# Optimization experiments

Measured on AMD Instinct MI355X. Metric: run time of the kernel, lower is better.

## Reference

```python
import jax, jax.numpy as jnp
import numpy as np

SCALES = (4, 8, 8)
PAD = 2
TOTAL = 256  # prod(SCALES) == frame shift
INDENT = PAD * TOTAL
BN_EPS = 1e-3  # keras BatchNormalization default


def _bn(x, g, b, m, v):
    return (x - m) * jax.lax.rsqrt(v + BN_EPS) * g + b


def _conv1d_valid(x, w):
    # x: [B, T, Cin], w: [K, Cin, Cout]
    return jax.lax.conv_general_dilated(x, w, (1,), 'VALID',
                                         dimension_numbers=('NWC', 'WIO', 'NWC'))


def _mel_conv_same(x, w):
    # per-mel-bin shared 1D conv along time. x: [B, T, M], w: [K]
    B, T, M = x.shape
    lhs = x.transpose(0, 2, 1).reshape(B * M, T, 1)
    rhs = w.reshape(-1, 1, 1)
    y = jax.lax.conv_general_dilated(lhs, rhs, (1,), 'SAME',
                                     dimension_numbers=('NWC', 'WIO', 'NWC'))
    return y.reshape(B, M, T).transpose(0, 2, 1)


def _gru(x, Wx, Wh, bx, bh):
    # keras GRUCell (reset_after=True): gate order z, r, h; h' = z*h + (1-z)*hh
    xp = x @ Wx + bx  # [B, T, 3H], input projection hoisted out of the scan
    H = Wh.shape[0]
    h0 = jnp.zeros((x.shape[0], H), x.dtype)

    def step(h, xt):
        rp = h @ Wh + bh
        xz, xr, xh = jnp.split(xt, 3, axis=-1)
        rz, rr, rh = jnp.split(rp, 3, axis=-1)
        z = jax.nn.sigmoid(xz + rz)
        r = jax.nn.sigmoid(xr + rr)
        hh = jnp.tanh(xh + r * rh)
        hn = z * h + (1.0 - z) * hh
        return hn, hn

    _, ys = jax.lax.scan(step, h0, xp.transpose(1, 0, 2))
    return ys.transpose(1, 0, 2)


def setup_inputs() -> dict:
    key = jax.random.key(0)
    ks = iter(jax.random.split(key, 64))
    B, T_MEL, M, C, H, R = 4, 44, 80, 128, 512, 10
    T_UP = TOTAL * (T_MEL - 2 * PAD)  # 10240
    s = 0.05
    d = {}
    d['audios'] = jax.random.normal(next(ks), (B, T_UP + 1), jnp.float32)
    d['mels'] = jax.random.normal(next(ks), (B, T_MEL, M), jnp.float32)
    d['w_mel0'] = jnp.full((2 * SCALES[0] + 1,), 1.0 / (2 * SCALES[0] + 1), jnp.float32)
    d['w_mel1'] = jnp.full((2 * SCALES[1] + 1,), 1.0 / (2 * SCALES[1] + 1), jnp.float32)
    d['w_mel2'] = jnp.full((2 * SCALES[2] + 1,), 1.0 / (2 * SCALES[2] + 1), jnp.float32)
    d['mr_conv0_w'] = jax.random.normal(next(ks), (5, M, C), jnp.float32) * s
    d['mr_bn0_g'] = jax.random.uniform(next(ks), (C,), jnp.float32, 0.5, 1.5)
    d['mr_bn0_b'] = jax.random.normal(next(ks), (C,), jnp.float32) * s
    d['mr_bn0_m'] = jnp.zeros((C,), jnp.float32)
    d['mr_bn0_v'] = jnp.ones((C,), jnp.float32)
    d['r_w1'] = jax.random.normal(next(ks), (R, C, C), jnp.float32) * s
    d['r_bn1_g'] = jax.random.uniform(next(ks), (R, C), jnp.float32, 0.5, 1.5)
    d['r_bn1_b'] = jax.random.normal(next(ks), (R, C), jnp.float32) * s
    d['r_bn1_m'] = jnp.zeros((R, C), jnp.float32)
    d['r_bn1_v'] = jnp.ones((R, C), jnp.float32)
    d['r_w2'] = jax.random.normal(next(ks), (R, C, C), jnp.float32) * s
    d['r_bn2_g'] = jax.random.uniform(next(ks), (R, C), jnp.float32, 0.5, 1.5)
    d['r_bn2_b'] = jax.random.normal(next(ks), (R, C), jnp.float32) * s
    d['r_bn2_m'] = jnp.zeros((R, C), jnp.float32)
    d['r_bn2_v'] = jnp.ones((R, C), jnp.float32)
    d['mr_out_w'] = jax.random.normal(next(ks), (C, C), jnp.float32) * s
    d['mr_out_b'] = jnp.zeros((C,), jnp.float32)
    A4 = C // 4  # 32
    d['Wi'] = jax.random.normal(next(ks), (1 + M + A4, H), jnp.float32) * s
    d['bi'] = jnp.zeros((H,), jnp.float32)
    d['Wx0'] = jax.random.normal(next(ks), (H, 3 * H), jnp.float32) * s
    d['Wh0'] = jax.random.normal(next(ks), (H, 3 * H), jnp.float32) * s
    d['bx0'] = jnp.zeros((3 * H,), jnp.float32)
    d['bh0'] = jnp.zeros((3 * H,), jnp.float32)
    d['Wx1'] = jax.random.normal(next(ks), (H + A4, 3 * H), jnp.float32) * s
    d['Wh1'] = jax.random.normal(next(ks), (H, 3 * H), jnp.float32) * s
    d['bx1'] = jnp.zeros((3 * H,), jnp.float32)
    d['bh1'] = jnp.zeros((3 * H,), jnp.float32)
    d['Wd0'] = jax.random.normal(next(ks), (H + A4, H), jnp.float32) * s
    d['bd0'] = jnp.zeros((H,), jnp.float32)
    d['Wd1'] = jax.random.normal(next(ks), (H + A4, H), jnp.float32) * s
    d['bd1'] = jnp.zeros((H,), jnp.float32)
    d['Wp'] = jax.random.normal(next(ks), (H, 30), jnp.float32) * s
    d['bp'] = jnp.zeros((30,), jnp.float32)
    return d


def reference(audios, mels, w_mel0, w_mel1, w_mel2,
              mr_conv0_w, mr_bn0_g, mr_bn0_b, mr_bn0_m, mr_bn0_v,
              r_w1, r_bn1_g, r_bn1_b, r_bn1_m, r_bn1_v,
              r_w2, r_bn2_g, r_bn2_b, r_bn2_m, r_bn2_v,
              mr_out_w, mr_out_b, Wi, bi,
              Wx0, Wh0, bx0, bh0, Wx1, Wh1, bx1, bh1,
              Wd0, bd0, Wd1, bd1, Wp, bp):
    # ---- UpsampleNet mel branch: nearest upsample + smoothing conv per scale ----
    x = mels
    for w, scale in zip((w_mel0, w_mel1, w_mel2), SCALES):
        x = jnp.repeat(x, scale, axis=1)
        x = _mel_conv_same(x, w)
    mels_up = x[:, INDENT:-INDENT, :]  # [B, T_up, 80]

    # ---- UpsampleNet aux branch: MelResNet (inference BN) + nearest upsample ----
    a = jax.nn.relu(_bn(_conv1d_valid(mels, mr_conv0_w),
                        mr_bn0_g, mr_bn0_b, mr_bn0_m, mr_bn0_v))
    for i in range(r_w1.shape[0]):
        y = jax.nn.relu(_bn(a @ r_w1[i], r_bn1_g[i], r_bn1_b[i], r_bn1_m[i], r_bn1_v[i]))
        y = _bn(y @ r_w2[i], r_bn2_g[i], r_bn2_b[i], r_bn2_m[i], r_bn2_v[i])
        a = a + y
    a = a @ mr_out_w + mr_out_b
    aux = jnp.repeat(a, TOTAL, axis=1)  # [B, T_up, 128]
    a0, a1, a2, a3 = jnp.split(aux, 4, axis=-1)

    # ---- WaveRNN teacher-forced trunk ----
    x = jnp.concatenate([audios[:, :-1, None], mels_up, a0], axis=-1)
    x = x @ Wi + bi  # [B, T_up, 512]
    x = _gru(x, Wx0, Wh0, bx0, bh0) + x
    x = _gru(jnp.concatenate([x, a1], axis=-1), Wx1, Wh1, bx1, bh1) + x
    x = jax.nn.relu(jnp.concatenate([x, a2], axis=-1) @ Wd0 + bd0) + x
    x = jax.nn.relu(jnp.concatenate([x, a3], axis=-1) @ Wd1 + bd1) + x
    logits = x @ Wp + bp  # [B, T_up, 30] (MoL parameters)
    return logits
```

## Files before the change

kernel.cpp:

```cpp
#include <hip/hip_runtime.h>
#include <hip/hip_bf16.h>

#define T_SEQ 10240
#define GRU_W 8

typedef short bf16x8 __attribute__((ext_vector_type(8)));
typedef float f32x4 __attribute__((ext_vector_type(4)));

__device__ __forceinline__ float bf2f(unsigned short u) {
    return __uint_as_float(((unsigned int)u) << 16);
}

__global__ void upsample_kernel(const float* __restrict__ in, float* __restrict__ out,
                                const float* __restrict__ wk,
                                int B, int Tin, int Tout, int shift, int taps)
{
    int idx = blockIdx.x * blockDim.x + threadIdx.x;
    int total = B * Tout * 80;
    if (idx >= total) return;
    int m = idx % 80;
    int r = idx / 80;
    int t = r % Tout;
    int b = r / Tout;
    int s = taps >> 1;
    float acc = 0.f;
    for (int d = -s; d <= s; ++d) {
        int i = t + d;
        if (i >= 0 && i < Tout)
            acc += in[((size_t)b * Tin + (i >> shift)) * 80 + m] * wk[d + s];
    }
    out[idx] = acc;
}

__global__ __launch_bounds__(128) void conv0_kernel(
    const float* __restrict__ mels, const float* __restrict__ w,
    const float* __restrict__ g, const float* __restrict__ b,
    const float* __restrict__ m_, const float* __restrict__ v_,
    float* __restrict__ a)
{
    __shared__ float xin[400];
    int bt = blockIdx.x;
    int bb = bt / 40, t = bt % 40;
    int c = threadIdx.x;
    for (int idx = c; idx < 400; idx += 128)
        xin[idx] = mels[((size_t)bb * 44 + t + idx / 80) * 80 + (idx % 80)];
    __syncthreads();
    float s = 0.f;
    for (int q = 0; q < 400; ++q) s += xin[q] * w[q * 128 + c];
    s = (s - m_[c]) * rsqrtf(v_[c] + 1e-3f) * g[c] + b[c];
    a[bt * 128 + c] = fmaxf(s, 0.f);
}

__global__ __launch_bounds__(128) void resblock_kernel(
    const float* __restrict__ W1, const float* __restrict__ W2,
    const float* __restrict__ g1, const float* __restrict__ b1,
    const float* __restrict__ m1, const float* __restrict__ v1,
    const float* __restrict__ g2, const float* __restrict__ b2,
    const float* __restrict__ m2, const float* __restrict__ v2,
    float* __restrict__ a)
{
    __shared__ float ain[128], y1[128];
    int tok = blockIdx.x;
    int c = threadIdx.x;
    ain[c] = a[tok * 128 + c];
    __syncthreads();
    float s = 0.f;
    #pragma unroll 8
    for (int k = 0; k < 128; ++k) s += ain[k] * W1[k * 128 + c];
    s = (s - m1[c]) * rsqrtf(v1[c] + 1e-3f) * g1[c] + b1[c];
    y1[c] = fmaxf(s, 0.f);
    __syncthreads();
    float s2 = 0.f;
    #pragma unroll 8
    for (int k = 0; k < 128; ++k) s2 += y1[k] * W2[k * 128 + c];
    s2 = (s2 - m2[c]) * rsqrtf(v2[c] + 1e-3f) * g2[c] + b2[c];
    a[tok * 128 + c] = ain[c] + s2;
}

__global__ __launch_bounds__(128) void outmat_kernel(
    const float* __restrict__ W, const float* __restrict__ bias,
    const float* __restrict__ a, float* __restrict__ out)
{
    __shared__ float ain[128];
    int tok = blockIdx.x;
    int c = threadIdx.x;
    ain[c] = a[tok * 128 + c];
    __syncthreads();
    float s = 0.f;
    #pragma unroll 8
    for (int k = 0; k < 128; ++k) s += ain[k] * W[k * 128 + c];
    out[tok * 128 + c] = s + bias[c];
}

__device__ __forceinline__ float fetchA(int mode, int row, int k, int K,
    const float* audio, const float* melsup, const float* cond, const float* xA)
{
    if (k >= K) return 0.f;
    int b = row / T_SEQ;
    int t = row - b * T_SEQ;
    if (mode == 0) {
        if (k == 0) return audio[(size_t)b * (T_SEQ + 1) + t];
        if (k < 81) return melsup[((size_t)b * 11264 + 512 + t) * 80 + (k - 1)];
        return cond[((size_t)b * 40 + (t >> 8)) * 128 + (k - 81)];
    }
    if (k < 512) return xA[(size_t)row * 512 + k];
    int co = (mode == 2) ? 32 : (mode == 3) ? 64 : 96;
    return cond[((size_t)b * 40 + (t >> 8)) * 128 + co + (k - 512)];
}

__global__ __launch_bounds__(256) void gemm_big(
    int mode, int N, int K,
    const float* __restrict__ W, const float* __restrict__ bias1,
    const float* __restrict__ bias2,
    const float* __restrict__ audio, const float* __restrict__ melsup,
    const float* __restrict__ cond, const float* __restrict__ xA,
    const float* __restrict__ resid, float* __restrict__ outF,
    __hip_bfloat16* __restrict__ outB)
{
    __shared__ float As[16][68];
    __shared__ float Bs[16][68];
    const int tid = threadIdx.x;
    const int row0 = blockIdx.y * 64;
    const int col0 = blockIdx.x * 64;
    const int tx = tid & 15, ty = tid >> 4;
    float acc[4][4] = {};
    const int nkt = (K + 15) >> 4;
    for (int kt = 0; kt < nkt; ++kt) {
        const int kb = kt << 4;
        #pragma unroll
        for (int l = 0; l < 4; ++l) {
            int k = (tid >> 6) + l * 4;
            int m = tid & 63;
            float bv = 0.f;
            if (kb + k < K) bv = W[(size_t)(kb + k) * N + col0 + m];
            Bs[k][m] = bv;
        }
        if (mode != 0) {
            int m = tid >> 2, kq = tid & 3;
            int row = row0 + m;
            int k = kb + kq * 4;
            if (k + 3 < 512) {
                float4 v = *reinterpret_cast<const float4*>(xA + (size_t)row * 512 + k);
                As[kq * 4 + 0][m] = v.x; As[kq * 4 + 1][m] = v.y;
                As[kq * 4 + 2][m] = v.z; As[kq * 4 + 3][m] = v.w;
            } else {
                #pragma unroll
                for (int i = 0; i < 4; ++i)
                    As[kq * 4 + i][m] = fetchA(mode, row, k + i, K, audio, melsup, cond, xA);
            }
        } else {
            #pragma unroll
            for (int l = 0; l < 4; ++l) {
                int k = (tid >> 6) + l * 4;
                int m = tid & 63;
                As[k][m] = fetchA(0, row0 + m, kb + k, K, audio, melsup, cond, xA);
            }
        }
        __syncthreads();
        #pragma unroll
        for (int k = 0; k < 16; ++k) {
            float a0 = As[k][(ty << 2) + 0], a1 = As[k][(ty << 2) + 1];
            float a2 = As[k][(ty << 2) + 2], a3 = As[k][(ty << 2) + 3];
            float b0 = Bs[k][(tx << 2) + 0], b1 = Bs[k][(tx << 2) + 1];
            float b2 = Bs[k][(tx << 2) + 2], b3 = Bs[k][(tx << 2) + 3];
            acc[0][0] += a0 * b0; acc[0][1] += a0 * b1; acc[0][2] += a0 * b2; acc[0][3] += a0 * b3;
            acc[1][0] += a1 * b0; acc[1][1] += a1 * b1; acc[1][2] += a1 * b2; acc[1][3] += a1 * b3;
            acc[2][0] += a2 * b0; acc[2][1] += a2 * b1; acc[2][2] += a2 * b2; acc[2][3] += a2 * b3;
            acc[3][0] += a3 * b0; acc[3][1] += a3 * b1; acc[3][2] += a3 * b2; acc[3][3] += a3 * b3;
        }
        __syncthreads();
    }
    #pragma unroll
    for (int i = 0; i < 4; ++i) {
        int row = row0 + (ty << 2) + i;
        #pragma unroll
        for (int jt = 0; jt < 4; ++jt) {
            int col = col0 + (tx << 2) + jt;
            float v = acc[i][jt] + bias1[col];
            if (bias2 && col < 1024) v += bias2[col];
            if (mode == 0) {
                outF[(size_t)row * N + col] = v;
            } else if (mode <= 2) {
                outB[(size_t)row * 1536 + col] = __float2bfloat16(v);
            } else {
                v = fmaxf(v, 0.f) + resid[(size_t)row * 512 + col];
                outF[(size_t)row * 512 + col] = v;
            }
        }
    }
}

__global__ __launch_bounds__(256) void pack_wh_kernel(const float* __restrict__ Wh,
                                                      unsigned short* __restrict__ out)
{
    int gid = blockIdx.x * 256 + threadIdx.x;
    int l = gid & 63;
    int idx = gid >> 6;
    int kt = idx & 15; idx >>= 4;
    int g = idx % 3;
    int ww = idx / 3;
    int wg = ww >> 2, w = ww & 3;
    int n = g * 512 + wg * 64 + w * 16 + (l & 15);
    int k0 = kt * 32 + (l >> 4) * 8;
    unsigned short* dst = out + (size_t)gid * 8;
    #pragma unroll
    for (int i = 0; i < 8; ++i) {
        __hip_bfloat16 hv = __float2bfloat16(Wh[(size_t)(k0 + i) * 1536 + n]);
        dst[i] = *reinterpret_cast<unsigned short*>(&hv);
    }
}

__global__ __launch_bounds__(256, 1) void gru_mfma8(
    const unsigned short* __restrict__ wpack,
    const float* __restrict__ bh,
    const __hip_bfloat16* __restrict__ xp,
    float* __restrict__ xio,
    unsigned int* __restrict__ hpair,
    int T)
{
    __shared__ alignas(16) unsigned short h_sh[2][16 * 512];

    const int tid = threadIdx.x;
    const int wg = blockIdx.x;
    const int w = tid >> 6;
    const int l = tid & 63;

    bf16x8 wf[3][16];
    {
        const bf16x8* wp = reinterpret_cast<const bf16x8*>(wpack);
        const int wbase = (wg * 4 + w) * 3 * 1024;
        #pragma unroll
        for (int g = 0; g < 3; ++g)
            #pragma unroll
            for (int kt = 0; kt < 16; ++kt)
                wf[g][kt] = wp[wbase + (g * 16 + kt) * 64 + l];
    }

    {
        uint4* z = reinterpret_cast<uint4*>(&h_sh[0][0]);
        #pragma unroll
        for (int i = 0; i < 8; ++i) z[tid + 256 * i] = make_uint4(0, 0, 0, 0);
    }

    const int j = wg * 64 + w * 16 + (l & 15);
    const float bhh = bh[1024 + j];
    float hprev[4] = {0.f, 0.f, 0.f, 0.f};
    float xz_c[4], xr_c[4], xh_c[4], xv_c[4];
    if (l < 16) {
        #pragma unroll
        for (int b = 0; b < 4; ++b) {
            const size_t rb = (size_t)b * T;
            xz_c[b] = bf2f(*reinterpret_cast<const unsigned short*>(xp + rb * 1536 + j));
            xr_c[b] = bf2f(*reinterpret_cast<const unsigned short*>(xp + rb * 1536 + 512 + j));
            xh_c[b] = bf2f(*reinterpret_cast<const unsigned short*>(xp + rb * 1536 + 1024 + j));
            xv_c[b] = xio[rb * 512 + j];
        }
    }
    __syncthreads();

    const unsigned long long* hp64 = reinterpret_cast<const unsigned long long*>(hpair);
    const int pb = tid >> 6;
    const int pchunk = (tid & 63) ^ (pb & 7);

    for (int t = 0; t < T; ++t) {
        const int cur = t & 1, nxt = cur ^ 1;

        const unsigned long long* src = hp64 + (size_t)cur * 1024 + tid * 4;
        const unsigned tg = (unsigned)t & 0xffffu;
        unsigned long long u0 = __hip_atomic_load(src + 0, __ATOMIC_RELAXED, __HIP_MEMORY_SCOPE_AGENT);
        unsigned long long u1 = __hip_atomic_load(src + 1, __ATOMIC_RELAXED, __HIP_MEMORY_SCOPE_AGENT);
        unsigned long long u2 = __hip_atomic_load(src + 2, __ATOMIC_RELAXED, __HIP_MEMORY_SCOPE_AGENT);
        unsigned long long u3 = __hip_atomic_load(src + 3, __ATOMIC_RELAXED, __HIP_MEMORY_SCOPE_AGENT);
        while ((((unsigned)(u0 >> 16) & 0xffffu) != tg) | ((unsigned)(u0 >> 48) != tg) |
               (((unsigned)(u1 >> 16) & 0xffffu) != tg) | ((unsigned)(u1 >> 48) != tg) |
               (((unsigned)(u2 >> 16) & 0xffffu) != tg) | ((unsigned)(u2 >> 48) != tg) |
               (((unsigned)(u3 >> 16) & 0xffffu) != tg) | ((unsigned)(u3 >> 48) != tg)) {
            __builtin_amdgcn_s_sleep(1);
            u0 = __hip_atomic_load(src + 0, __ATOMIC_RELAXED, __HIP_MEMORY_SCOPE_AGENT);
            u1 = __hip_atomic_load(src + 1, __ATOMIC_RELAXED, __HIP_MEMORY_SCOPE_AGENT);
            u2 = __hip_atomic_load(src + 2, __ATOMIC_RELAXED, __HIP_MEMORY_SCOPE_AGENT);
            u3 = __hip_atomic_load(src + 3, __ATOMIC_RELAXED, __HIP_MEMORY_SCOPE_AGENT);
        }
        {
            uint4 wv;
            wv.x = (unsigned)(u0 & 0xffffull) | ((unsigned)((u0 >> 32) & 0xffffull) << 16);
            wv.y = (unsigned)(u1 & 0xffffull) | ((unsigned)((u1 >> 32) & 0xffffull) << 16);
            wv.z = (unsigned)(u2 & 0xffffull) | ((unsigned)((u2 >> 32) & 0xffffull) << 16);
            wv.w = (unsigned)(u3 & 0xffffull) | ((unsigned)((u3 >> 32) & 0xffffull) << 16);
            *reinterpret_cast<uint4*>(
                reinterpret_cast<char*>(&h_sh[cur][0]) + pb * 1024 + pchunk * 16) = wv;
        }
        __syncthreads();

        f32x4 acc0 = {0, 0, 0, 0}, acc1 = {0, 0, 0, 0}, acc2 = {0, 0, 0, 0};
        const int rb = l & 15, q = l >> 4;
        const char* hb = reinterpret_cast<const char*>(&h_sh[cur][0]);
        #pragma unroll
        for (int kt = 0; kt < 16; ++kt) {
            bf16x8 afr = *reinterpret_cast<const bf16x8*>(
                hb + rb * 1024 + ((((kt * 4 + q) ^ (rb & 7))) << 4));
            acc0 = __builtin_amdgcn_mfma_f32_16x16x32_bf16(afr, wf[0][kt], acc0, 0, 0, 0);
            acc1 = __builtin_amdgcn_mfma_f32_16x16x32_bf16(afr, wf[1][kt], acc1, 0, 0, 0);
            acc2 = __builtin_amdgcn_mfma_f32_16x16x32_bf16(afr, wf[2][kt], acc2, 0, 0, 0);
        }

        if (l < 16) {
            float hn[4];
            #pragma unroll
            for (int b = 0; b < 4; ++b) {
                float z = 1.f / (1.f + __expf(-(xz_c[b] + acc0[b])));
                float r = 1.f / (1.f + __expf(-(xr_c[b] + acc1[b])));
                float e2 = __expf(-2.f * (xh_c[b] + r * (acc2[b] + bhh)));
                float hh = (1.f - e2) / (1.f + e2);
                hn[b] = z * hprev[b] + (1.f - z) * hh;
                hprev[b] = hn[b];
            }
            if (t + 1 < T) {
                const unsigned ptag = (unsigned)((t + 1) & 0xffff) << 16;
                #pragma unroll
                for (int b = 0; b < 4; ++b) {
                    __hip_bfloat16 hb16 = __float2bfloat16(hn[b]);
                    __hip_atomic_store(hpair + (size_t)nxt * 2048 + b * 512 + j,
                                       ptag | (unsigned)*reinterpret_cast<unsigned short*>(&hb16),
                                       __ATOMIC_RELAXED, __HIP_MEMORY_SCOPE_AGENT);
                }
            }
            #pragma unroll
            for (int b = 0; b < 4; ++b)
                xio[((size_t)b * T + t) * 512 + j] = xv_c[b] + hn[b];
            if (t + 1 < T) {
                #pragma unroll
                for (int b = 0; b < 4; ++b) {
                    const size_t rb2 = (size_t)b * T + t + 1;
                    xz_c[b] = bf2f(*reinterpret_cast<const unsigned short*>(xp + rb2 * 1536 + j));
                    xr_c[b] = bf2f(*reinterpret_cast<const unsigned short*>(xp + rb2 * 1536 + 512 + j));
                    xh_c[b] = bf2f(*reinterpret_cast<const unsigned short*>(xp + rb2 * 1536 + 1024 + j));
                    xv_c[b] = xio[rb2 * 512 + j];
                }
            }
        }
    }
}

__global__ __launch_bounds__(256) void wp_kernel(
    const float* __restrict__ x, const float* __restrict__ Wp,
    const float* __restrict__ bp, float* __restrict__ out)
{
    int r = threadIdx.x >> 5, c = threadIdx.x & 31;
    size_t row = (size_t)blockIdx.x * 8 + r;
    if (c >= 30) return;
    const float* xr = x + row * 512;
    float acc = 0.f;
    #pragma unroll 8
    for (int k = 0; k < 512; ++k) acc += xr[k] * Wp[k * 30 + c];
    out[row * 30 + c] = acc + bp[c];
}

extern "C" void kernel_launch(void* const* d_in, const int* in_sizes, int n_in,
                              void* d_out, int out_size, void* d_ws, size_t ws_size,
                              hipStream_t stream)
{
    const float* audios = (const float*)d_in[0];
    const float* mels   = (const float*)d_in[1];
    const float* w_mel0 = (const float*)d_in[2];
    const float* w_mel1 = (const float*)d_in[3];
    const float* w_mel2 = (const float*)d_in[4];
    const float* conv0w = (const float*)d_in[5];
    const float* bn0g = (const float*)d_in[6];
    const float* bn0b = (const float*)d_in[7];
    const float* bn0m = (const float*)d_in[8];
    const float* bn0v = (const float*)d_in[9];
    const float* r_w1   = (const float*)d_in[10];
    const float* r_bn1g = (const float*)d_in[11];
    const float* r_bn1b = (const float*)d_in[12];
    const float* r_bn1m = (const float*)d_in[13];
    const float* r_bn1v = (const float*)d_in[14];
    const float* r_w2   = (const float*)d_in[15];
    const float* r_bn2g = (const float*)d_in[16];
    const float* r_bn2b = (const float*)d_in[17];
    const float* r_bn2m = (const float*)d_in[18];
    const float* r_bn2v = (const float*)d_in[19];
    const float* mr_out_w = (const float*)d_in[20];
    const float* mr_out_b = (const float*)d_in[21];
    const float* Wi = (const float*)d_in[22];
    const float* bi = (const float*)d_in[23];
    const float* Wx0 = (const float*)d_in[24];
    const float* Wh0 = (const float*)d_in[25];
    const float* bx0 = (const float*)d_in[26];
    const float* bh0 = (const float*)d_in[27];
    const float* Wx1 = (const float*)d_in[28];
    const float* Wh1 = (const float*)d_in[29];
    const float* bx1 = (const float*)d_in[30];
    const float* bh1 = (const float*)d_in[31];
    const float* Wd0 = (const float*)d_in[32];
    const float* bd0 = (const float*)d_in[33];
    const float* Wd1 = (const float*)d_in[34];
    const float* bd1 = (const float*)d_in[35];
    const float* Wp = (const float*)d_in[36];
    const float* bp = (const float*)d_in[37];

    char* ws = (char*)d_ws;
    size_t off = 0;
    auto alloc = [&](size_t n) { size_t r = off; off += (n + 255) & ~(size_t)255; return r; };
    const size_t M = 4 * (size_t)T_SEQ;
    size_t xp_off = alloc(M * 1536 * 2);
    size_t x_off  = alloc(M * 512 * 4);
    size_t s1_off = alloc((size_t)4 * 176 * 80 * 4);
    size_t s2_off = alloc((size_t)4 * 1408 * 80 * 4);
    size_t s3_off = alloc((size_t)4 * 11264 * 80 * 4);
    size_t ca_off = alloc((size_t)160 * 128 * 4);
    size_t cf_off = alloc((size_t)160 * 128 * 4);
    size_t wp0_off = alloc((size_t)98304 * 8 * 2);
    size_t wp1_off = alloc((size_t)98304 * 8 * 2);
    size_t hp_off  = alloc(2 * 2048 * 4);

    __hip_bfloat16* xp = (__hip_bfloat16*)(ws + xp_off);
    float* x3   = (float*)(ws + xp_off);
    float* xbuf = (float*)(ws + x_off);
    float* st1  = (float*)(ws + s1_off);
    float* st2  = (float*)(ws + s2_off);
    float* st3  = (float*)(ws + s3_off);
    float* conda = (float*)(ws + ca_off);
    float* condf = (float*)(ws + cf_off);
    unsigned short* wpack0 = (unsigned short*)(ws + wp0_off);
    unsigned short* wpack1 = (unsigned short*)(ws + wp1_off);
    unsigned int* hpair = (unsigned int*)(ws + hp_off);
    float* outp = (float*)d_out;

    pack_wh_kernel<<<384, 256, 0, stream>>>(Wh0, wpack0);
    pack_wh_kernel<<<384, 256, 0, stream>>>(Wh1, wpack1);

    {
        int tot1 = 4 * 176 * 80;
        upsample_kernel<<<(tot1 + 255) / 256, 256, 0, stream>>>(mels, st1, w_mel0, 4, 44, 176, 2, 9);
        int tot2 = 4 * 1408 * 80;
        upsample_kernel<<<(tot2 + 255) / 256, 256, 0, stream>>>(st1, st2, w_mel1, 4, 176, 1408, 3, 17);
        int tot3 = 4 * 11264 * 80;
        upsample_kernel<<<(tot3 + 255) / 256, 256, 0, stream>>>(st2, st3, w_mel2, 4, 1408, 11264, 3, 17);
    }
    conv0_kernel<<<160, 128, 0, stream>>>(mels, conv0w, bn0g, bn0b, bn0m, bn0v, conda);
    for (int i = 0; i < 10; ++i) {
        resblock_kernel<<<160, 128, 0, stream>>>(
            r_w1 + (size_t)i * 128 * 128, r_w2 + (size_t)i * 128 * 128,
            r_bn1g + i * 128, r_bn1b + i * 128, r_bn1m + i * 128, r_bn1v + i * 128,
            r_bn2g + i * 128, r_bn2b + i * 128, r_bn2m + i * 128, r_bn2v + i * 128,
            conda);
    }
    outmat_kernel<<<160, 128, 0, stream>>>(mr_out_w, mr_out_b, conda, condf);

    dim3 blk(256);
    gemm_big<<<dim3(8, 640), blk, 0, stream>>>(0, 512, 113, Wi, bi, nullptr,
        audios, st3, condf, nullptr, nullptr, xbuf, nullptr);
    gemm_big<<<dim3(24, 640), blk, 0, stream>>>(1, 1536, 512, Wx0, bx0, bh0,
        nullptr, nullptr, condf, xbuf, nullptr, nullptr, xp);
    hipMemsetAsync(ws + hp_off, 0, 2 * 2048 * 4, stream);
    gru_mfma8<<<GRU_W, 256, 0, stream>>>(wpack0, bh0, xp, xbuf, hpair, T_SEQ);
    gemm_big<<<dim3(24, 640), blk, 0, stream>>>(2, 1536, 544, Wx1, bx1, bh1,
        nullptr, nullptr, condf, xbuf, nullptr, nullptr, xp);
    hipMemsetAsync(ws + hp_off, 0, 2 * 2048 * 4, stream);
    gru_mfma8<<<GRU_W, 256, 0, stream>>>(wpack1, bh1, xp, xbuf, hpair, T_SEQ);
    gemm_big<<<dim3(8, 640), blk, 0, stream>>>(3, 512, 544, Wd0, bd0, nullptr,
        nullptr, nullptr, condf, xbuf, xbuf, x3, nullptr);
    gemm_big<<<dim3(8, 640), blk, 0, stream>>>(4, 512, 544, Wd1, bd1, nullptr,
        nullptr, nullptr, condf, x3, x3, xbuf, nullptr);
    wp_kernel<<<5120, 256, 0, stream>>>(xbuf, Wp, bp, outp);
}
```

Before: 48.35 ms.

## Fuse both GRU layers into one pipelined persistent kernel with in-loop input projection

Replaces the two sequential GRU launches and their two big input-projection GEMMs with a single 16-block persistent kernel. Layer 0 and layer 1 run concurrently, with layer 1 consuming layer 0 outputs through a tagged ring buffer and a progress counter that bounds the lag. Each block adds four extra waves that compute the x@Wx projection per timestep with MFMA. The per-frame conditioning part of layer 1 is precomputed by a small kernel. This removes the GEMM passes and the xp round-trip through memory and overlaps the two recurrences. In exchange the per-step critical path gets longer, there is more block-to-block synchronisation, and layer-0 outputs are now rounded to bf16.

```diff
diff --git a/kernel.cpp b/kernel.cpp
--- a/kernel.cpp
+++ b/kernel.cpp
@@ -2,13 +2,16 @@
 #include <hip/hip_bf16.h>
 
 #define T_SEQ 10240
-#define GRU_W 8
 
 typedef short bf16x8 __attribute__((ext_vector_type(8)));
 typedef float f32x4 __attribute__((ext_vector_type(4)));
 
 __device__ __forceinline__ float bf2f(unsigned short u) {
     return __uint_as_float(((unsigned int)u) << 16);
+}
+__device__ __forceinline__ unsigned short f2bf(float f) {
+    __hip_bfloat16 h = __float2bfloat16(f);
+    return *reinterpret_cast<unsigned short*>(&h);
 }
 
 __global__ void upsample_kernel(const float* __restrict__ in, float* __restrict__ out,
@@ -104,14 +107,13 @@
         return cond[((size_t)b * 40 + (t >> 8)) * 128 + (k - 81)];
     }
     if (k < 512) return xA[(size_t)row * 512 + k];
-    int co = (mode == 2) ? 32 : (mode == 3) ? 64 : 96;
+    int co = (mode == 3) ? 64 : 96;
     return cond[((size_t)b * 40 + (t >> 8)) * 128 + co + (k - 512)];
 }
 
 __global__ __launch_bounds__(256) void gemm_big(
     int mode, int N, int K,
     const float* __restrict__ W, const float* __restrict__ bias1,
-    const float* __restrict__ bias2,
     const float* __restrict__ audio, const float* __restrict__ melsup,
     const float* __restrict__ cond, const float* __restrict__ xA,
     const float* __restrict__ resid, float* __restrict__ outF,
@@ -177,11 +179,8 @@
         for (int jt = 0; jt < 4; ++jt) {
             int col = col0 + (tx << 2) + jt;
             float v = acc[i][jt] + bias1[col];
-            if (bias2 && col < 1024) v += bias2[col];
             if (mode == 0) {
-                outF[(size_t)row * N + col] = v;
-            } else if (mode <= 2) {
-                outB[(size_t)row * 1536 + col] = __float2bfloat16(v);
+                outB[(size_t)row * 512 + col] = __float2bfloat16(v);
             } else {
                 v = fmaxf(v, 0.f) + resid[(size_t)row * 512 + col];
                 outF[(size_t)row * 512 + col] = v;
@@ -190,127 +189,232 @@
     }
 }
 
-__global__ __launch_bounds__(256) void pack_wh_kernel(const float* __restrict__ Wh,
-                                                      unsigned short* __restrict__ out)
-{
-    int gid = blockIdx.x * 256 + threadIdx.x;
-    int l = gid & 63;
-    int idx = gid >> 6;
+__global__ __launch_bounds__(256) void pack_w_kernel(const float* __restrict__ Wh,
+                                                     const float* __restrict__ Wx,
+                                                     unsigned short* __restrict__ out)
+{
+    int F = blockIdx.x * 256 + threadIdx.x;
+    int l = F & 63;
+    int idx = F >> 6;
     int kt = idx & 15; idx >>= 4;
-    int g = idx % 3;
-    int ww = idx / 3;
-    int wg = ww >> 2, w = ww & 3;
-    int n = g * 512 + wg * 64 + w * 16 + (l & 15);
+    int g = idx % 3; idx /= 3;
+    int w = idx & 7;
+    int wg = idx >> 3;
+    const float* src = (w < 4) ? Wh : Wx;
+    int uw = w & 3;
+    int n = g * 512 + wg * 64 + uw * 16 + (l & 15);
     int k0 = kt * 32 + (l >> 4) * 8;
-    unsigned short* dst = out + (size_t)gid * 8;
+    unsigned short* dst = out + (size_t)F * 8;
     #pragma unroll
-    for (int i = 0; i < 8; ++i) {
-        __hip_bfloat16 hv = __float2bfloat16(Wh[(size_t)(k0 + i) * 1536 + n]);
-        dst[i] = *reinterpret_cast<unsigned short*>(&hv);
-    }
-}
-
-__global__ __launch_bounds__(256, 1) void gru_mfma8(
+    for (int i = 0; i < 8; ++i)
+        dst[i] = f2bf(src[(size_t)(k0 + i) * 1536 + n]);
+}
+
+__global__ __launch_bounds__(256) void xa1_kernel(const float* __restrict__ Wx1,
+                                                  const float* __restrict__ bx1,
+                                                  const float* __restrict__ bh1,
+                                                  const float* __restrict__ cond,
+                                                  float* __restrict__ xa1)
+{
+    int idx = blockIdx.x * 256 + threadIdx.x;
+    if (idx >= 245760) return;
+    int n = idx % 1536;
+    int bf = idx / 1536;
+    float s = bx1[n] + (n < 1024 ? bh1[n] : 0.f);
+    const float* a = cond + (size_t)bf * 128 + 32;
+    #pragma unroll 8
+    for (int k = 0; k < 32; ++k) s += a[k] * Wx1[(size_t)(512 + k) * 1536 + n];
+    xa1[idx] = s;
+}
+
+__global__ __launch_bounds__(512, 1) void gru_fused(
     const unsigned short* __restrict__ wpack,
-    const float* __restrict__ bh,
-    const __hip_bfloat16* __restrict__ xp,
+    const float* __restrict__ bx0, const float* __restrict__ bh0,
+    const float* __restrict__ bh1,
+    const float* __restrict__ xa1,
+    const __hip_bfloat16* __restrict__ xb16,
     float* __restrict__ xio,
-    unsigned int* __restrict__ hpair,
+    unsigned int* __restrict__ hr0,
+    unsigned int* __restrict__ hr1,
+    unsigned int* __restrict__ x1r,
+    unsigned int* __restrict__ prog,
     int T)
 {
-    __shared__ alignas(16) unsigned short h_sh[2][16 * 512];
+    __shared__ alignas(16) unsigned short h_sh[16 * 512];
+    __shared__ alignas(16) unsigned short x_sh[3][16 * 512];
+    __shared__ alignas(16) float accx[4][16][3][4];
+    __shared__ alignas(16) float xab[4][16][3][4];
 
     const int tid = threadIdx.x;
-    const int wg = blockIdx.x;
-    const int w = tid >> 6;
-    const int l = tid & 63;
+    const int layer = blockIdx.x >> 3, wg = blockIdx.x & 7;
+    const int w = tid >> 6, l = tid & 63;
+    const bool ish = (w < 4);
+    const int uw = w & 3;
 
     bf16x8 wf[3][16];
     {
         const bf16x8* wp = reinterpret_cast<const bf16x8*>(wpack);
-        const int wbase = (wg * 4 + w) * 3 * 1024;
+        const size_t base = (size_t)layer * 196608 + (size_t)((wg * 8 + w) * 3) * 16 * 64;
         #pragma unroll
         for (int g = 0; g < 3; ++g)
             #pragma unroll
             for (int kt = 0; kt < 16; ++kt)
-                wf[g][kt] = wp[wbase + (g * 16 + kt) * 64 + l];
+                wf[g][kt] = wp[base + (g * 16 + kt) * 64 + l];
     }
 
     {
-        uint4* z = reinterpret_cast<uint4*>(&h_sh[0][0]);
-        #pragma unroll
-        for (int i = 0; i < 8; ++i) z[tid + 256 * i] = make_uint4(0, 0, 0, 0);
-    }
-
-    const int j = wg * 64 + w * 16 + (l & 15);
-    const float bhh = bh[1024 + j];
+        uint4* z1 = reinterpret_cast<uint4*>(h_sh);
+        for (int i = tid; i < 1024; i += 512) z1[i] = make_uint4(0, 0, 0, 0);
+        uint4* z2 = reinterpret_cast<uint4*>(&x_sh[0][0]);
+        for (int i = tid; i < 3072; i += 512) z2[i] = make_uint4(0, 0, 0, 0);
+    }
+
+    const int j = wg * 64 + uw * 16 + (l & 15);
+    float bhh = 0.f;
     float hprev[4] = {0.f, 0.f, 0.f, 0.f};
-    float xz_c[4], xr_c[4], xh_c[4], xv_c[4];
-    if (l < 16) {
+    if (ish && l < 16)
+        bhh = (layer == 0) ? bh0[1024 + j] : bh1[1024 + j];
+    __syncthreads();
+
+    if (ish && l < 16 && layer == 0) {
         #pragma unroll
         for (int b = 0; b < 4; ++b) {
-            const size_t rb = (size_t)b * T;
-            xz_c[b] = bf2f(*reinterpret_cast<const unsigned short*>(xp + rb * 1536 + j));
-            xr_c[b] = bf2f(*reinterpret_cast<const unsigned short*>(xp + rb * 1536 + 512 + j));
-            xh_c[b] = bf2f(*reinterpret_cast<const unsigned short*>(xp + rb * 1536 + 1024 + j));
-            xv_c[b] = xio[rb * 512 + j];
-        }
-    }
-    __syncthreads();
-
-    const unsigned long long* hp64 = reinterpret_cast<const unsigned long long*>(hpair);
-    const int pb = tid >> 6;
-    const int pchunk = (tid & 63) ^ (pb & 7);
+            xab[w][l][0][b] = bx0[j] + bh0[j];
+            xab[w][l][1][b] = bx0[512 + j] + bh0[512 + j];
+            xab[w][l][2][b] = bx0[1024 + j];
+        }
+    }
+
+    const int xc = tid & 255;
+    const int xb = xc >> 6, xch = xc & 63;
+    uint4 xhold = make_uint4(0, 0, 0, 0);
+    if (!ish && layer == 0) {
+        uint4 v0 = *reinterpret_cast<const uint4*>(
+            reinterpret_cast<const unsigned short*>(xb16) + ((size_t)xb * T) * 512 + xch * 8);
+        *reinterpret_cast<uint4*>(
+            reinterpret_cast<char*>(&x_sh[0][0]) + xb * 1024 + ((xch ^ (xb & 7))) * 16) = v0;
+        int t1 = (T > 1) ? 1 : 0;
+        xhold = *reinterpret_cast<const uint4*>(
+            reinterpret_cast<const unsigned short*>(xb16) + ((size_t)xb * T + t1) * 512 + xch * 8);
+    }
+
+    unsigned int* hr = layer ? hr1 : hr0;
+    const unsigned long long* hr64 = reinterpret_cast<const unsigned long long*>(hr);
+    const unsigned long long* xr64 = reinterpret_cast<const unsigned long long*>(x1r);
 
     for (int t = 0; t < T; ++t) {
-        const int cur = t & 1, nxt = cur ^ 1;
-
-        const unsigned long long* src = hp64 + (size_t)cur * 1024 + tid * 4;
-        const unsigned tg = (unsigned)t & 0xffffu;
-        unsigned long long u0 = __hip_atomic_load(src + 0, __ATOMIC_RELAXED, __HIP_MEMORY_SCOPE_AGENT);
-        unsigned long long u1 = __hip_atomic_load(src + 1, __ATOMIC_RELAXED, __HIP_MEMORY_SCOPE_AGENT);
-        unsigned long long u2 = __hip_atomic_load(src + 2, __ATOMIC_RELAXED, __HIP_MEMORY_SCOPE_AGENT);
-        unsigned long long u3 = __hip_atomic_load(src + 3, __ATOMIC_RELAXED, __HIP_MEMORY_SCOPE_AGENT);
-        while ((((unsigned)(u0 >> 16) & 0xffffu) != tg) | ((unsigned)(u0 >> 48) != tg) |
-               (((unsigned)(u1 >> 16) & 0xffffu) != tg) | ((unsigned)(u1 >> 48) != tg) |
-               (((unsigned)(u2 >> 16) & 0xffffu) != tg) | ((unsigned)(u2 >> 48) != tg) |
-               (((unsigned)(u3 >> 16) & 0xffffu) != tg) | ((unsigned)(u3 >> 48) != tg)) {
-            __builtin_amdgcn_s_sleep(1);
-            u0 = __hip_atomic_load(src + 0, __ATOMIC_RELAXED, __HIP_MEMORY_SCOPE_AGENT);
-            u1 = __hip_atomic_load(src + 1, __ATOMIC_RELAXED, __HIP_MEMORY_SCOPE_AGENT);
-            u2 = __hip_atomic_load(src + 2, __ATOMIC_RELAXED, __HIP_MEMORY_SCOPE_AGENT);
-            u3 = __hip_atomic_load(src + 3, __ATOMIC_RELAXED, __HIP_MEMORY_SCOPE_AGENT);
-        }
-        {
+        const int cur = t & 1;
+        const int xbuf = t % 3;
+        unsigned pg0 = 0;
+
+        if (ish) {
+            if (layer == 0 && l < 16)
+                pg0 = __hip_atomic_load(prog + (l & 7) * 16, __ATOMIC_RELAXED, __HIP_MEMORY_SCOPE_AGENT);
+            const unsigned long long* src = hr64 + (size_t)cur * 1024 + tid * 4;
+            const unsigned tg = (unsigned)t & 0xffffu;
+            unsigned long long u0 = __hip_atomic_load(src + 0, __ATOMIC_RELAXED, __HIP_MEMORY_SCOPE_AGENT);
+            unsigned long long u1 = __hip_atomic_load(src + 1, __ATOMIC_RELAXED, __HIP_MEMORY_SCOPE_AGENT);
+            unsigned long long u2 = __hip_atomic_load(src + 2, __ATOMIC_RELAXED, __HIP_MEMORY_SCOPE_AGENT);
+            unsigned long long u3 = __hip_atomic_load(src + 3, __ATOMIC_RELAXED, __HIP_MEMORY_SCOPE_AGENT);
+            while ((((unsigned)(u0 >> 16) & 0xffffu) != tg) | ((unsigned)(u0 >> 48) != tg) |
+                   (((unsigned)(u1 >> 16) & 0xffffu) != tg) | ((unsigned)(u1 >> 48) != tg) |
+                   (((unsigned)(u2 >> 16) & 0xffffu) != tg) | ((unsigned)(u2 >> 48) != tg) |
+                   (((unsigned)(u3 >> 16) & 0xffffu) != tg) | ((unsigned)(u3 >> 48) != tg)) {
+                __builtin_amdgcn_s_sleep(1);
+                u0 = __hip_atomic_load(src + 0, __ATOMIC_RELAXED, __HIP_MEMORY_SCOPE_AGENT);
+                u1 = __hip_atomic_load(src + 1, __ATOMIC_RELAXED, __HIP_MEMORY_SCOPE_AGENT);
+                u2 = __hip_atomic_load(src + 2, __ATOMIC_RELAXED, __HIP_MEMORY_SCOPE_AGENT);
+                u3 = __hip_atomic_load(src + 3, __ATOMIC_RELAXED, __HIP_MEMORY_SCOPE_AGENT);
+            }
             uint4 wv;
             wv.x = (unsigned)(u0 & 0xffffull) | ((unsigned)((u0 >> 32) & 0xffffull) << 16);
             wv.y = (unsigned)(u1 & 0xffffull) | ((unsigned)((u1 >> 32) & 0xffffull) << 16);
             wv.z = (unsigned)(u2 & 0xffffull) | ((unsigned)((u2 >> 32) & 0xffffull) << 16);
             wv.w = (unsigned)(u3 & 0xffffull) | ((unsigned)((u3 >> 32) & 0xffffull) << 16);
             *reinterpret_cast<uint4*>(
-                reinterpret_cast<char*>(&h_sh[cur][0]) + pb * 1024 + pchunk * 16) = wv;
+                reinterpret_cast<char*>(h_sh) + (tid >> 6) * 1024 +
+                (((tid & 63) ^ ((tid >> 6) & 7))) * 16) = wv;
+        } else {
+            if (layer == 0) {
+                *reinterpret_cast<uint4*>(
+                    reinterpret_cast<char*>(&x_sh[(t + 1) % 3][0]) + xb * 1024 +
+                    ((xch ^ (xb & 7))) * 16) = xhold;
+                int tn = (t + 2 < T) ? t + 2 : T - 1;
+                xhold = *reinterpret_cast<const uint4*>(
+                    reinterpret_cast<const unsigned short*>(xb16) +
+                    ((size_t)xb * T + tn) * 512 + xch * 8);
+            } else {
+                const unsigned long long* src = xr64 + (size_t)(t & 31) * 1024 + xc * 4;
+                const unsigned tg = (unsigned)(t + 1) & 0xffffu;
+                unsigned long long u0 = __hip_atomic_load(src + 0, __ATOMIC_RELAXED, __HIP_MEMORY_SCOPE_AGENT);
+                unsigned long long u1 = __hip_atomic_load(src + 1, __ATOMIC_RELAXED, __HIP_MEMORY_SCOPE_AGENT);
+                unsigned long long u2 = __hip_atomic_load(src + 2, __ATOMIC_RELAXED, __HIP_MEMORY_SCOPE_AGENT);
+                unsigned long long u3 = __hip_atomic_load(src + 3, __ATOMIC_RELAXED, __HIP_MEMORY_SCOPE_AGENT);
+                while ((((unsigned)(u0 >> 16) & 0xffffu) != tg) | ((unsigned)(u0 >> 48) != tg) |
+                       (((unsigned)(u1 >> 16) & 0xffffu) != tg) | ((unsigned)(u1 >> 48) != tg) |
+                       (((unsigned)(u2 >> 16) & 0xffffu) != tg) | ((unsigned)(u2 >> 48) != tg) |
+                       (((unsigned)(u3 >> 16) & 0xffffu) != tg) | ((unsigned)(u3 >> 48) != tg)) {
+                    __builtin_amdgcn_s_sleep(1);
+                    u0 = __hip_atomic_load(src + 0, __ATOMIC_RELAXED, __HIP_MEMORY_SCOPE_AGENT);
+                    u1 = __hip_atomic_load(src + 1, __ATOMIC_RELAXED, __HIP_MEMORY_SCOPE_AGENT);
+                    u2 = __hip_atomic_load(src + 2, __ATOMIC_RELAXED, __HIP_MEMORY_SCOPE_AGENT);
+                    u3 = __hip_atomic_load(src + 3, __ATOMIC_RELAXED, __HIP_MEMORY_SCOPE_AGENT);
+                }
+                uint4 wv;
+                wv.x = (unsigned)(u0 & 0xffffull) | ((unsigned)((u0 >> 32) & 0xffffull) << 16);
+                wv.y = (unsigned)(u1 & 0xffffull) | ((unsigned)((u1 >> 32) & 0xffffull) << 16);
+                wv.z = (unsigned)(u2 & 0xffffull) | ((unsigned)((u2 >> 32) & 0xffffull) << 16);
+                wv.w = (unsigned)(u3 & 0xffffull) | ((unsigned)((u3 >> 32) & 0xffffull) << 16);
+                *reinterpret_cast<uint4*>(
+                    reinterpret_cast<char*>(&x_sh[xbuf][0]) + xb * 1024 +
+                    ((xch ^ (xb & 7))) * 16) = wv;
+            }
         }
         __syncthreads();
 
-        f32x4 acc0 = {0, 0, 0, 0}, acc1 = {0, 0, 0, 0}, acc2 = {0, 0, 0, 0};
+        const char* A = ish ? reinterpret_cast<const char*>(h_sh)
+                            : reinterpret_cast<const char*>(&x_sh[xbuf][0]);
+        f32x4 a0 = {0, 0, 0, 0}, a1 = {0, 0, 0, 0}, a2 = {0, 0, 0, 0};
         const int rb = l & 15, q = l >> 4;
-        const char* hb = reinterpret_cast<const char*>(&h_sh[cur][0]);
         #pragma unroll
         for (int kt = 0; kt < 16; ++kt) {
             bf16x8 afr = *reinterpret_cast<const bf16x8*>(
-                hb + rb * 1024 + ((((kt * 4 + q) ^ (rb & 7))) << 4));
-            acc0 = __builtin_amdgcn_mfma_f32_16x16x32_bf16(afr, wf[0][kt], acc0, 0, 0, 0);
-            acc1 = __builtin_amdgcn_mfma_f32_16x16x32_bf16(afr, wf[1][kt], acc1, 0, 0, 0);
-            acc2 = __builtin_amdgcn_mfma_f32_16x16x32_bf16(afr, wf[2][kt], acc2, 0, 0, 0);
-        }
-
-        if (l < 16) {
-            float hn[4];
+                A + rb * 1024 + ((((kt * 4 + q) ^ (rb & 7))) << 4));
+            a0 = __builtin_amdgcn_mfma_f32_16x16x32_bf16(afr, wf[0][kt], a0, 0, 0, 0);
+            a1 = __builtin_amdgcn_mfma_f32_16x16x32_bf16(afr, wf[1][kt], a1, 0, 0, 0);
+            a2 = __builtin_amdgcn_mfma_f32_16x16x32_bf16(afr, wf[2][kt], a2, 0, 0, 0);
+        }
+        if (!ish && l < 16) {
+            *reinterpret_cast<f32x4*>(&accx[uw][l][0][0]) = a0;
+            *reinterpret_cast<f32x4*>(&accx[uw][l][1][0]) = a1;
+            *reinterpret_cast<f32x4*>(&accx[uw][l][2][0]) = a2;
+        }
+        __syncthreads();
+
+        if (ish && l < 16) {
+            if (layer == 1 && (t & 255) == 0) {
+                const int f = t >> 8;
+                #pragma unroll
+                for (int b = 0; b < 4; ++b) {
+                    const size_t base = (size_t)(b * 40 + f) * 1536;
+                    xab[w][l][0][b] = xa1[base + j];
+                    xab[w][l][1][b] = xa1[base + 512 + j];
+                    xab[w][l][2][b] = xa1[base + 1024 + j];
+                }
+            }
+            float hn[4], xv[4];
             #pragma unroll
             for (int b = 0; b < 4; ++b) {
-                float z = 1.f / (1.f + __expf(-(xz_c[b] + acc0[b])));
-                float r = 1.f / (1.f + __expf(-(xr_c[b] + acc1[b])));
-                float e2 = __expf(-2.f * (xh_c[b] + r * (acc2[b] + bhh)));
+                const unsigned short xu = *reinterpret_cast<const unsigned short*>(
+                    reinterpret_cast<const char*>(&x_sh[xbuf][0]) + b * 1024 +
+                    (((j >> 3) ^ (b & 7)) << 4) + (j & 7) * 2);
+                xv[b] = bf2f(xu);
+                float xz_ = accx[w][l][0][b] + xab[w][l][0][b];
+                float xr_ = accx[w][l][1][b] + xab[w][l][1][b];
+                float xh_ = accx[w][l][2][b] + xab[w][l][2][b];
+                float z = 1.f / (1.f + __expf(-(xz_ + a0[b])));
+                float r = 1.f / (1.f + __expf(-(xr_ + a1[b])));
+                float e2 = __expf(-2.f * (xh_ + r * (a2[b] + bhh)));
                 float hh = (1.f - e2) / (1.f + e2);
                 hn[b] = z * hprev[b] + (1.f - z) * hh;
                 hprev[b] = hn[b];
@@ -318,25 +422,29 @@
             if (t + 1 < T) {
                 const unsigned ptag = (unsigned)((t + 1) & 0xffff) << 16;
                 #pragma unroll
-                for (int b = 0; b < 4; ++b) {
-                    __hip_bfloat16 hb16 = __float2bfloat16(hn[b]);
-                    __hip_atomic_store(hpair + (size_t)nxt * 2048 + b * 512 + j,
-                                       ptag | (unsigned)*reinterpret_cast<unsigned short*>(&hb16),
+                for (int b = 0; b < 4; ++b)
+                    __hip_atomic_store(hr + (size_t)((t + 1) & 1) * 2048 + b * 512 + j,
+                                       ptag | (unsigned)f2bf(hn[b]),
                                        __ATOMIC_RELAXED, __HIP_MEMORY_SCOPE_AGENT);
+            }
+            if (layer == 0) {
+                while ((int)t - (int)pg0 > 24) {
+                    __builtin_amdgcn_s_sleep(8);
+                    pg0 = __hip_atomic_load(prog + (l & 7) * 16, __ATOMIC_RELAXED, __HIP_MEMORY_SCOPE_AGENT);
                 }
-            }
-            #pragma unroll
-            for (int b = 0; b < 4; ++b)
-                xio[((size_t)b * T + t) * 512 + j] = xv_c[b] + hn[b];
-            if (t + 1 < T) {
+                const unsigned xtag = (unsigned)((t + 1) & 0xffff) << 16;
                 #pragma unroll
-                for (int b = 0; b < 4; ++b) {
-                    const size_t rb2 = (size_t)b * T + t + 1;
-                    xz_c[b] = bf2f(*reinterpret_cast<const unsigned short*>(xp + rb2 * 1536 + j));
-                    xr_c[b] = bf2f(*reinterpret_cast<const unsigned short*>(xp + rb2 * 1536 + 512 + j));
-                    xh_c[b] = bf2f(*reinterpret_cast<const unsigned short*>(xp + rb2 * 1536 + 1024 + j));
-                    xv_c[b] = xio[rb2 * 512 + j];
-                }
+                for (int b = 0; b < 4; ++b)
+                    __hip_atomic_store(x1r + (size_t)(t & 31) * 2048 + b * 512 + j,
+                                       xtag | (unsigned)f2bf(xv[b] + hn[b]),
+                                       __ATOMIC_RELAXED, __HIP_MEMORY_SCOPE_AGENT);
+            } else {
+                #pragma unroll
+                for (int b = 0; b < 4; ++b)
+                    xio[((size_t)b * T + t) * 512 + j] = xv[b] + hn[b];
+                if (w == 0 && l == 0)
+                    __hip_atomic_store(prog + wg * 16, (unsigned)t,
+                                       __ATOMIC_RELAXED, __HIP_MEMORY_SCOPE_AGENT);
             }
         }
     }
@@ -403,41 +511,41 @@
     size_t off = 0;
     auto alloc = [&](size_t n) { size_t r = off; off += (n + 255) & ~(size_t)255; return r; };
     const size_t M = 4 * (size_t)T_SEQ;
-    size_t xp_off = alloc(M * 1536 * 2);
-    size_t x_off  = alloc(M * 512 * 4);
+    size_t x3_off  = alloc(M * 512 * 4);
+    size_t xio_off = alloc(M * 512 * 4);
+    size_t xb_off  = alloc(M * 512 * 2);
     size_t s1_off = alloc((size_t)4 * 176 * 80 * 4);
     size_t s2_off = alloc((size_t)4 * 1408 * 80 * 4);
     size_t s3_off = alloc((size_t)4 * 11264 * 80 * 4);
     size_t ca_off = alloc((size_t)160 * 128 * 4);
     size_t cf_off = alloc((size_t)160 * 128 * 4);
-    size_t wp0_off = alloc((size_t)98304 * 8 * 2);
-    size_t wp1_off = alloc((size_t)98304 * 8 * 2);
-    size_t hp_off  = alloc(2 * 2048 * 4);
-
-    __hip_bfloat16* xp = (__hip_bfloat16*)(ws + xp_off);
-    float* x3   = (float*)(ws + xp_off);
-    float* xbuf = (float*)(ws + x_off);
+    size_t wp_off = alloc((size_t)2 * 196608 * 8 * 2);
+    size_t xa_off = alloc((size_t)245760 * 4);
+    size_t rg_off = alloc(16384 + 16384 + 262144 + 512);
+
+    float* x3   = (float*)(ws + x3_off);
+    float* xio  = (float*)(ws + xio_off);
+    __hip_bfloat16* xb16 = (__hip_bfloat16*)(ws + xb_off);
     float* st1  = (float*)(ws + s1_off);
     float* st2  = (float*)(ws + s2_off);
     float* st3  = (float*)(ws + s3_off);
     float* conda = (float*)(ws + ca_off);
     float* condf = (float*)(ws + cf_off);
-    unsigned short* wpack0 = (unsigned short*)(ws + wp0_off);
-    unsigned short* wpack1 = (unsigned short*)(ws + wp1_off);
-    unsigned int* hpair = (unsigned int*)(ws + hp_off);
+    unsigned short* wpack = (unsigned short*)(ws + wp_off);
+    float* xa1 = (float*)(ws + xa_off);
+    unsigned int* hr0 = (unsigned int*)(ws + rg_off);
+    unsigned int* hr1 = (unsigned int*)(ws + rg_off + 16384);
+    unsigned int* x1r = (unsigned int*)(ws + rg_off + 32768);
+    unsigned int* prog = (unsigned int*)(ws + rg_off + 32768 + 262144);
     float* outp = (float*)d_out;
 
-    pack_wh_kernel<<<384, 256, 0, stream>>>(Wh0, wpack0);
-    pack_wh_kernel<<<384, 256, 0, stream>>>(Wh1, wpack1);
-
-    {
-        int tot1 = 4 * 176 * 80;
-        upsample_kernel<<<(tot1 + 255) / 256, 256, 0, stream>>>(mels, st1, w_mel0, 4, 44, 176, 2, 9);
-        int tot2 = 4 * 1408 * 80;
-        upsample_kernel<<<(tot2 + 255) / 256, 256, 0, stream>>>(st1, st2, w_mel1, 4, 176, 1408, 3, 17);
-        int tot3 = 4 * 11264 * 80;
-        upsample_kernel<<<(tot3 + 255) / 256, 256, 0, stream>>>(st2, st3, w_mel2, 4, 1408, 11264, 3, 17);
-    }
+    pack_w_kernel<<<768, 256, 0, stream>>>(Wh0, Wx0, wpack);
+    pack_w_kernel<<<768, 256, 0, stream>>>(Wh1, Wx1, wpack + (size_t)196608 * 8);
+
+    upsample_kernel<<<(4 * 176 * 80 + 255) / 256, 256, 0, stream>>>(mels, st1, w_mel0, 4, 44, 176, 2, 9);
+    upsample_kernel<<<(4 * 1408 * 80 + 255) / 256, 256, 0, stream>>>(st1, st2, w_mel1, 4, 176, 1408, 3, 17);
+    upsample_kernel<<<(4 * 11264 * 80 + 255) / 256, 256, 0, stream>>>(st2, st3, w_mel2, 4, 1408, 11264, 3, 17);
+
     conv0_kernel<<<160, 128, 0, stream>>>(mels, conv0w, bn0g, bn0b, bn0m, bn0v, conda);
     for (int i = 0; i < 10; ++i) {
         resblock_kernel<<<160, 128, 0, stream>>>(
@@ -448,20 +556,18 @@
     }
     outmat_kernel<<<160, 128, 0, stream>>>(mr_out_w, mr_out_b, conda, condf);
 
-    dim3 blk(256);
-    gemm_big<<<dim3(8, 640), blk, 0, stream>>>(0, 512, 113, Wi, bi, nullptr,
-        audios, st3, condf, nullptr, nullptr, xbuf, nullptr);
-    gemm_big<<<dim3(24, 640), blk, 0, stream>>>(1, 1536, 512, Wx0, bx0, bh0,
-        nullptr, nullptr, condf, xbuf, nullptr, nullptr, xp);
-    hipMemsetAsync(ws + hp_off, 0, 2 * 2048 * 4, stream);
-    gru_mfma8<<<GRU_W, 256, 0, stream>>>(wpack0, bh0, xp, xbuf, hpair, T_SEQ);
-    gemm_big<<<dim3(24, 640), blk, 0, stream>>>(2, 1536, 544, Wx1, bx1, bh1,
-        nullptr, nullptr, condf, xbuf, nullptr, nullptr, xp);
-    hipMemsetAsync(ws + hp_off, 0, 2 * 2048 * 4, stream);
-    gru_mfma8<<<GRU_W, 256, 0, stream>>>(wpack1, bh1, xp, xbuf, hpair, T_SEQ);
-    gemm_big<<<dim3(8, 640), blk, 0, stream>>>(3, 512, 544, Wd0, bd0, nullptr,
-        nullptr, nullptr, condf, xbuf, xbuf, x3, nullptr);
-    gemm_big<<<dim3(8, 640), blk, 0, stream>>>(4, 512, 544, Wd1, bd1, nullptr,
-        nullptr, nullptr, condf, x3, x3, xbuf, nullptr);
-    wp_kernel<<<5120, 256, 0, stream>>>(xbuf, Wp, bp, outp);
-}
+    xa1_kernel<<<960, 256, 0, stream>>>(Wx1, bx1, bh1, condf, xa1);
+
+    gemm_big<<<dim3(8, 640), 256, 0, stream>>>(0, 512, 113, Wi, bi,
+        audios, st3, condf, nullptr, nullptr, nullptr, xb16);
+
+    hipMemsetAsync(ws + rg_off, 0, 16384 + 16384 + 262144 + 512, stream);
+    gru_fused<<<16, 512, 0, stream>>>(wpack, bx0, bh0, bh1, xa1, xb16, xio,
+                                      hr0, hr1, x1r, prog, T_SEQ);
+
+    gemm_big<<<dim3(8, 640), 256, 0, stream>>>(3, 512, 544, Wd0, bd0,
+        nullptr, nullptr, condf, xio, xio, x3, nullptr);
+    gemm_big<<<dim3(8, 640), 256, 0, stream>>>(4, 512, 544, Wd1, bd1,
+        nullptr, nullptr, condf, x3, x3, xio, nullptr);
+    wp_kernel<<<5120, 256, 0, stream>>>(xio, Wp, bp, outp);
+}
```

Measured after the change: 49.56 ms. 2.5% more time.
